# Kernel tuning notes

Hardware: AMD Instinct MI355X
Metric: run time of the kernel (lower is better)

Reference implementation:

```python
import jax, jax.numpy as jnp
import numpy as np

N_NODES = 50000


def setup_inputs() -> dict:
    key = jax.random.key(0)
    k1, k2, k3, k4 = jax.random.split(key, 4)
    in_c, hid = 256, 128
    x = jax.random.normal(k1, (N_NODES, in_c), dtype=jnp.float32)
    edge_index = jax.random.randint(k2, (2, 800000), 0, N_NODES, dtype=jnp.int32)
    # GCNConv weight (glorot) and bias
    W_conv = jax.random.normal(k3, (in_c, hid), dtype=jnp.float32) * (1.0 / np.sqrt(in_c))
    b_conv = jnp.zeros((hid,), dtype=jnp.float32)
    # Final Linear (xavier_uniform per reset_parameters)
    limit = np.sqrt(6.0 / (hid + in_c))
    W_lin = jax.random.uniform(k4, (hid, in_c), dtype=jnp.float32, minval=-limit, maxval=limit)
    b_lin = jnp.zeros((in_c,), dtype=jnp.float32)
    return {"x": x, "edge_index": edge_index, "W_conv": W_conv, "b_conv": b_conv,
            "W_lin": W_lin, "b_lin": b_lin}


def _gcn_conv(x, edge_index, W, b):
    n = x.shape[0]
    # add self-loops (standard GCN normalization)
    loop = jnp.arange(n, dtype=edge_index.dtype)
    src = jnp.concatenate([edge_index[0], loop])
    dst = jnp.concatenate([edge_index[1], loop])
    # transform first (in_c -> hid) so the edge gather moves the smaller dim
    h = x @ W  # [N, hid]
    deg = jax.ops.segment_sum(jnp.ones_like(dst, dtype=h.dtype), dst, num_segments=n)
    dinv = jnp.where(deg > 0, jax.lax.rsqrt(deg), 0.0)
    norm = dinv[src] * dinv[dst]  # [E+N]
    msg = h[src] * norm[:, None]  # [E+N, hid]
    out = jax.ops.segment_sum(msg, dst, num_segments=n)
    return out + b


def reference(x, edge_index, W_conv, b_conv, W_lin, b_lin):
    h = _gcn_conv(x, edge_index, W_conv, b_conv)  # [N, hid]
    # dropout p=0.0 -> identity
    return h @ W_lin + b_lin  # [N, in_c]
```

## Files before the change

kernel.cpp:

```cpp
#include <hip/hip_runtime.h>
#include <hip/hip_fp16.h>


#define N_NODES 50000
#define N_EDGES 800000
#define IN_C 256
#define HID 128
#define SCAN_BLOCKS ((N_NODES + 255) / 256)
#define GEMM_MBLK ((N_NODES + 63) / 64)
#define PREP_BLOCKS 1024
#define BUCKET_BLOCKS 2048
#define LDK 72

#define OFF_H    0UL
#define OFF_CONV 12800000UL
#define OFF_DEG  25600000UL
#define OFF_RP   25800000UL
#define OFF_DINV 26000064UL
#define OFF_RANK 26200064UL
#define OFF_REC  27800064UL
#define OFF_BSUM 31000064UL
#define OFF_WT1  31001088UL
#define OFF_WT2  31066624UL

typedef __attribute__((ext_vector_type(8))) short bf16x8;
typedef __attribute__((ext_vector_type(4))) float f32x4;

__device__ __forceinline__ ushort f2bf(float x) {
    unsigned u = __float_as_uint(x);
    u += 0x7fffu + ((u >> 16) & 1u);
    return (ushort)(u >> 16);
}

__global__ __launch_bounds__(256) void prep_kernel(
    const float* __restrict__ Wc, const float* __restrict__ Wl,
    ushort* __restrict__ wtc, ushort* __restrict__ wtl,
    const int* __restrict__ dst, ushort* __restrict__ rank, int* __restrict__ deg)
{
    int i = blockIdx.x * 256 + threadIdx.x;
    if (i < HID * IN_C) {
        int n = i / IN_C, k = i % IN_C;
        wtc[i] = f2bf(Wc[k * HID + n]);
    } else if (i < 2 * HID * IN_C) {
        int j = i - HID * IN_C;
        int n = j / HID, k = j % HID;
        wtl[j] = f2bf(Wl[k * IN_C + n]);
    }
    for (int e = i; e < N_EDGES; e += PREP_BLOCKS * 256)
        rank[e] = (ushort)atomicAdd(&deg[dst[e]], 1);
}

__global__ __launch_bounds__(256) void scan_blocks_kernel(
    const int* __restrict__ deg, int* __restrict__ row_ptr,
    int* __restrict__ bsums, int n)
{
    __shared__ int tmp[256];
    int tid = threadIdx.x;
    int i = blockIdx.x * 256 + tid;
    int v = (i < n) ? deg[i] : 0;
    int orig = v;
    tmp[tid] = v;
    __syncthreads();
    #pragma unroll
    for (int off = 1; off < 256; off <<= 1) {
        int t = (tid >= off) ? tmp[tid - off] : 0;
        __syncthreads();
        tmp[tid] += t;
        __syncthreads();
    }
    if (i < n) row_ptr[i] = tmp[tid] - orig;
    if (tid == 255) bsums[blockIdx.x] = tmp[255];
}

__global__ __launch_bounds__(256) void finalize2_kernel(
    const int* __restrict__ deg, int* __restrict__ row_ptr,
    const int* __restrict__ bsums, float* __restrict__ dinv, int n)
{
    __shared__ int tmp[256];
    __shared__ int orig[256];
    int tid = threadIdx.x;
    int v = (tid < SCAN_BLOCKS) ? bsums[tid] : 0;
    tmp[tid] = v;
    orig[tid] = v;
    __syncthreads();
    #pragma unroll
    for (int off = 1; off < 256; off <<= 1) {
        int t = (tid >= off) ? tmp[tid - off] : 0;
        __syncthreads();
        tmp[tid] += t;
        __syncthreads();
    }
    int boff = tmp[blockIdx.x] - orig[blockIdx.x];
    int i = blockIdx.x * 256 + tid;
    if (i < n) {
        row_ptr[i] += boff;
        dinv[i] = rsqrtf((float)(deg[i] + 1));
    }
    if (i == 0) row_ptr[n] = N_EDGES;
}

__global__ __launch_bounds__(256) void bucket_kernel(
    const int* __restrict__ src, const int* __restrict__ dst,
    const ushort* __restrict__ rank, const int* __restrict__ row_ptr,
    const float* __restrict__ dinv, unsigned* __restrict__ rec)
{
    int cls = blockIdx.x & 7;
    int blk = blockIdx.x >> 3;
    int lo = cls * (N_NODES / 8);
    int hi = lo + (N_NODES / 8);
    const int CHUNK = (N_EDGES + 255) / 256;
    int e0 = blk * CHUNK;
    int e1 = min(e0 + CHUNK, N_EDGES);
    for (int i = e0 + threadIdx.x; i < e1; i += 256) {
        int d = dst[i];
        if (d >= lo && d < hi) {
            int s = src[i];
            unsigned r = (unsigned)(ushort)s |
                         ((unsigned)__half_as_ushort(__float2half_rn(dinv[s])) << 16);
            rec[row_ptr[d] + rank[i]] = r;
        }
    }
}

template <int KT, bool A_IS_BF16, bool BF16OUT>
__global__ __launch_bounds__(256) void mfma_gemm_kernel(
    const void* __restrict__ Av, const ushort* __restrict__ Bt,
    const float* __restrict__ bias, void* __restrict__ Cv,
    int M, int N)
{
    constexpr int NIT = KT / 64;
    __shared__ __align__(16) ushort As[64 * LDK];
    __shared__ __align__(16) ushort Bs[128 * LDK];
    int tid = threadIdx.x;
    int wave = tid >> 6, lane = tid & 63;
    int quad = lane >> 4, l16 = lane & 15;
    int wm0 = (wave >> 1) * 32, wn0 = (wave & 1) * 64;
    int bm = blockIdx.x * 64, bn = blockIdx.y * 128;

    int arow = tid >> 2, acol = (tid & 3) * 16;
    int agrow = bm + arow;
    int brow = tid >> 1, bkk = (tid & 1) * 32;

    f32x4 acc[2][4] = {};
    float4 a32[2][4];
    bf16x8 a16[2][2];
    bf16x8 breg[2][4];

    auto issue = [&](int it, int s) {
        int k0 = it * 64;
        if (A_IS_BF16) {
            a16[s][0] = bf16x8{};
            a16[s][1] = bf16x8{};
            if (agrow < M) {
                const ushort* ap = (const ushort*)Av + (size_t)agrow * KT + k0 + acol;
                a16[s][0] = *(const bf16x8*)ap;
                a16[s][1] = *(const bf16x8*)(ap + 8);
            }
        } else {
            a32[s][0] = a32[s][1] = a32[s][2] = a32[s][3] = make_float4(0.f, 0.f, 0.f, 0.f);
            if (agrow < M) {
                const float* ap = (const float*)Av + (size_t)agrow * KT + k0 + acol;
                a32[s][0] = *(const float4*)ap;
                a32[s][1] = *(const float4*)(ap + 4);
                a32[s][2] = *(const float4*)(ap + 8);
                a32[s][3] = *(const float4*)(ap + 12);
            }
        }
        const ushort* bp = Bt + (size_t)(bn + brow) * KT + k0 + bkk;
        breg[s][0] = *(const bf16x8*)bp;
        breg[s][1] = *(const bf16x8*)(bp + 8);
        breg[s][2] = *(const bf16x8*)(bp + 16);
        breg[s][3] = *(const bf16x8*)(bp + 24);
    };

    auto stage = [&](int s) {
        if (A_IS_BF16) {
            *(bf16x8*)&As[arow * LDK + acol]     = a16[s][0];
            *(bf16x8*)&As[arow * LDK + acol + 8] = a16[s][1];
        } else {
            ushort t0[8] = {f2bf(a32[s][0].x), f2bf(a32[s][0].y), f2bf(a32[s][0].z), f2bf(a32[s][0].w),
                            f2bf(a32[s][1].x), f2bf(a32[s][1].y), f2bf(a32[s][1].z), f2bf(a32[s][1].w)};
            ushort t1[8] = {f2bf(a32[s][2].x), f2bf(a32[s][2].y), f2bf(a32[s][2].z), f2bf(a32[s][2].w),
                            f2bf(a32[s][3].x), f2bf(a32[s][3].y), f2bf(a32[s][3].z), f2bf(a32[s][3].w)};
            *(bf16x8*)&As[arow * LDK + acol]     = *(bf16x8*)t0;
            *(bf16x8*)&As[arow * LDK + acol + 8] = *(bf16x8*)t1;
        }
        *(bf16x8*)&Bs[brow * LDK + bkk]      = breg[s][0];
        *(bf16x8*)&Bs[brow * LDK + bkk + 8]  = breg[s][1];
        *(bf16x8*)&Bs[brow * LDK + bkk + 16] = breg[s][2];
        *(bf16x8*)&Bs[brow * LDK + bkk + 24] = breg[s][3];
    };

    issue(0, 0);
    #pragma unroll
    for (int it = 0; it < NIT; ++it) {
        int cur = it & 1;
        if (it + 1 < NIT) issue(it + 1, cur ^ 1);
        if (it > 0) __syncthreads();
        stage(cur);
        __syncthreads();
        bf16x8 af[2][2], bfr[4][2];
        #pragma unroll
        for (int im = 0; im < 2; ++im)
            #pragma unroll
            for (int kh = 0; kh < 2; ++kh)
                af[im][kh] = *(bf16x8*)&As[(wm0 + im * 16 + l16) * LDK + kh * 32 + quad * 8];
        #pragma unroll
        for (int in = 0; in < 4; ++in)
            #pragma unroll
            for (int kh = 0; kh < 2; ++kh)
                bfr[in][kh] = *(bf16x8*)&Bs[(wn0 + in * 16 + l16) * LDK + kh * 32 + quad * 8];
        #pragma unroll
        for (int im = 0; im < 2; ++im)
            #pragma unroll
            for (int in = 0; in < 4; ++in) {
                acc[im][in] = __builtin_amdgcn_mfma_f32_16x16x32_bf16(
                    af[im][0], bfr[in][0], acc[im][in], 0, 0, 0);
                acc[im][in] = __builtin_amdgcn_mfma_f32_16x16x32_bf16(
                    af[im][1], bfr[in][1], acc[im][in], 0, 0, 0);
            }
    }
    #pragma unroll
    for (int im = 0; im < 2; ++im) {
        #pragma unroll
        for (int in = 0; in < 4; ++in) {
            int col = bn + wn0 + in * 16 + l16;
            float bval = bias ? bias[col] : 0.f;
            #pragma unroll
            for (int r = 0; r < 4; ++r) {
                int grow = bm + wm0 + im * 16 + quad * 4 + r;
                if (grow < M) {
                    float o = acc[im][in][r] + bval;
                    if (BF16OUT)
                        ((ushort*)Cv)[(size_t)grow * N + col] = f2bf(o);
                    else
                        ((float*)Cv)[(size_t)grow * N + col] = o;
                }
            }
        }
    }
}

__device__ __forceinline__ void acc_edge(float4& acc, unsigned r,
                                         const ushort* __restrict__ hb, int c) {
    unsigned s = r & 0xffffu;
    float w = __half2float(__ushort_as_half((ushort)(r >> 16)));
    uint2 v = *(const uint2*)&hb[(size_t)s * HID + c];
    acc.x += w * __uint_as_float(v.x << 16);
    acc.y += w * __uint_as_float(v.x & 0xffff0000u);
    acc.z += w * __uint_as_float(v.y << 16);
    acc.w += w * __uint_as_float(v.y & 0xffff0000u);
}

__global__ __launch_bounds__(256, 4) void gather_kernel(
    const ushort* __restrict__ hb, const int* __restrict__ row_ptr,
    const unsigned* __restrict__ rec, const float* __restrict__ dinv,
    const float* __restrict__ b_conv, ushort* __restrict__ convb, int n)
{
    int wave = threadIdx.x >> 6;
    int lane = threadIdx.x & 63;
    int d = blockIdx.x * 4 + wave;
    if (d >= n) return;
    int half = lane >> 5;
    int l32 = lane & 31;
    int c = l32 << 2;

    float4 acc = make_float4(0.f, 0.f, 0.f, 0.f);
    int begin = row_ptr[d], end = row_ptr[d + 1];
    int e = begin + half;
    for (; e + 14 < end; e += 16) {
        unsigned r0 = rec[e];
        unsigned r1 = rec[e + 2];
        unsigned r2 = rec[e + 4];
        unsigned r3 = rec[e + 6];
        unsigned r4 = rec[e + 8];
        unsigned r5 = rec[e + 10];
        unsigned r6 = rec[e + 12];
        unsigned r7 = rec[e + 14];
        acc_edge(acc, r0, hb, c);
        acc_edge(acc, r1, hb, c);
        acc_edge(acc, r2, hb, c);
        acc_edge(acc, r3, hb, c);
        acc_edge(acc, r4, hb, c);
        acc_edge(acc, r5, hb, c);
        acc_edge(acc, r6, hb, c);
        acc_edge(acc, r7, hb, c);
    }
    for (; e + 6 < end; e += 8) {
        unsigned r0 = rec[e];
        unsigned r1 = rec[e + 2];
        unsigned r2 = rec[e + 4];
        unsigned r3 = rec[e + 6];
        acc_edge(acc, r0, hb, c);
        acc_edge(acc, r1, hb, c);
        acc_edge(acc, r2, hb, c);
        acc_edge(acc, r3, hb, c);
    }
    for (; e < end; e += 2) {
        unsigned r0 = rec[e];
        acc_edge(acc, r0, hb, c);
    }
    acc.x += __shfl_xor(acc.x, 32);
    acc.y += __shfl_xor(acc.y, 32);
    acc.z += __shfl_xor(acc.z, 32);
    acc.w += __shfl_xor(acc.w, 32);

    if (half == 0) {
        float di = dinv[d];
        uint2 hv = *(const uint2*)&hb[(size_t)d * HID + c];
        acc.x += di * __uint_as_float(hv.x << 16);
        acc.y += di * __uint_as_float(hv.x & 0xffff0000u);
        acc.z += di * __uint_as_float(hv.y << 16);
        acc.w += di * __uint_as_float(hv.y & 0xffff0000u);
        float4 bb = *(const float4*)&b_conv[c];
        float ox = di * acc.x + bb.x;
        float oy = di * acc.y + bb.y;
        float oz = di * acc.z + bb.z;
        float ow = di * acc.w + bb.w;
        uint2 po;
        po.x = ((unsigned)f2bf(oy) << 16) | (unsigned)f2bf(ox);
        po.y = ((unsigned)f2bf(ow) << 16) | (unsigned)f2bf(oz);
        *(uint2*)&convb[(size_t)d * HID + c] = po;
    }
}

extern "C" void kernel_launch(void* const* d_in, const int* in_sizes, int n_in,
                              void* d_out, int out_size, void* d_ws, size_t ws_size,
                              hipStream_t stream) {
    const float* x      = (const float*)d_in[0];
    const int*   ei     = (const int*)d_in[1];
    const float* W_conv = (const float*)d_in[2];
    const float* b_conv = (const float*)d_in[3];
    const float* W_lin  = (const float*)d_in[4];
    const float* b_lin  = (const float*)d_in[5];
    float* out = (float*)d_out;

    char* ws = (char*)d_ws;
    ushort* hb      = (ushort*)(ws + OFF_H);
    ushort* convb   = (ushort*)(ws + OFF_CONV);
    int*    deg     = (int*)(ws + OFF_DEG);
    int*    row_ptr = (int*)(ws + OFF_RP);
    float*  dinv    = (float*)(ws + OFF_DINV);
    ushort* rank    = (ushort*)(ws + OFF_RANK);
    unsigned* rec   = (unsigned*)(ws + OFF_REC);
    int*    bsums   = (int*)(ws + OFF_BSUM);
    ushort* wt_conv = (ushort*)(ws + OFF_WT1);
    ushort* wt_lin  = (ushort*)(ws + OFF_WT2);

    const int* src = ei;
    const int* dst = ei + N_EDGES;

    hipMemsetAsync(deg, 0, 200000, stream);

    prep_kernel<<<PREP_BLOCKS, 256, 0, stream>>>(W_conv, W_lin, wt_conv, wt_lin,
                                                 dst, rank, deg);
    scan_blocks_kernel<<<SCAN_BLOCKS, 256, 0, stream>>>(deg, row_ptr, bsums, N_NODES);
    finalize2_kernel<<<SCAN_BLOCKS, 256, 0, stream>>>(deg, row_ptr, bsums, dinv, N_NODES);

    bucket_kernel<<<BUCKET_BLOCKS, 256, 0, stream>>>(src, dst, rank, row_ptr, dinv, rec);

    mfma_gemm_kernel<IN_C, false, true><<<dim3(GEMM_MBLK, HID / 128), 256, 0, stream>>>(
        x, wt_conv, nullptr, hb, N_NODES, HID);

    gather_kernel<<<(N_NODES + 3) / 4, 256, 0, stream>>>(
        hb, row_ptr, rec, dinv, b_conv, convb, N_NODES);

    mfma_gemm_kernel<HID, true, false><<<dim3(GEMM_MBLK, IN_C / 128), 256, 0, stream>>>(
        convb, wt_lin, b_lin, out, N_NODES, IN_C);
}
```

Baseline: 229.9 us.

## Fuse degree scan, finalize and bucket into one CSR-building kernel

Replaces the two-kernel block scan plus bucket kernel with one csr_kernel. Each block redundantly computes the prefix sum for its 1/8 node class in shared memory, then scatters edge records using the shared-memory row pointers. The dinv array is dropped and rsqrt(deg+1) is recomputed on the fly. This removes two launches and the global row_ptr and dinv round trips. The cost is that every one of the 2048 blocks redundantly re-reads and reduces up to 50000 degrees.

```diff
diff --git a/kernel.cpp b/kernel.cpp
--- a/kernel.cpp
+++ b/kernel.cpp
@@ -6,10 +6,10 @@
 #define N_EDGES 800000
 #define IN_C 256
 #define HID 128
-#define SCAN_BLOCKS ((N_NODES + 255) / 256)
 #define GEMM_MBLK ((N_NODES + 63) / 64)
 #define PREP_BLOCKS 1024
-#define BUCKET_BLOCKS 2048
+#define CSR_BLOCKS 2048
+#define CSIZE (N_NODES / 8)
 #define LDK 72
 
 #define OFF_H    0UL
@@ -50,16 +50,40 @@
         rank[e] = (ushort)atomicAdd(&deg[dst[e]], 1);
 }
 
-__global__ __launch_bounds__(256) void scan_blocks_kernel(
-    const int* __restrict__ deg, int* __restrict__ row_ptr,
-    int* __restrict__ bsums, int n)
+__global__ __launch_bounds__(256) void csr_kernel(
+    const int* __restrict__ src, const int* __restrict__ dst,
+    const ushort* __restrict__ rank, const int* __restrict__ deg,
+    int* __restrict__ row_ptr, unsigned* __restrict__ rec)
 {
+    __shared__ int rp[CSIZE];
     __shared__ int tmp[256];
     int tid = threadIdx.x;
-    int i = blockIdx.x * 256 + tid;
-    int v = (i < n) ? deg[i] : 0;
-    int orig = v;
-    tmp[tid] = v;
+    int cls = blockIdx.x & 7;
+    int blk = blockIdx.x >> 3;
+    int lo = cls * CSIZE;
+
+    int sum = 0;
+    for (int i = tid; i < lo; i += 256) sum += deg[i];
+    tmp[tid] = sum;
+    __syncthreads();
+    #pragma unroll
+    for (int off = 128; off > 0; off >>= 1) {
+        if (tid < off) tmp[tid] += tmp[tid + off];
+        __syncthreads();
+    }
+    int base = tmp[0];
+    __syncthreads();
+
+    int vals[25];
+    int tsum = 0;
+    if (tid < 250) {
+        #pragma unroll
+        for (int j = 0; j < 25; ++j) {
+            vals[j] = deg[lo + tid * 25 + j];
+            tsum += vals[j];
+        }
+    }
+    tmp[tid] = tsum;
     __syncthreads();
     #pragma unroll
     for (int off = 1; off < 256; off <<= 1) {
@@ -68,56 +92,34 @@
         tmp[tid] += t;
         __syncthreads();
     }
-    if (i < n) row_ptr[i] = tmp[tid] - orig;
-    if (tid == 255) bsums[blockIdx.x] = tmp[255];
-}
-
-__global__ __launch_bounds__(256) void finalize2_kernel(
-    const int* __restrict__ deg, int* __restrict__ row_ptr,
-    const int* __restrict__ bsums, float* __restrict__ dinv, int n)
-{
-    __shared__ int tmp[256];
-    __shared__ int orig[256];
-    int tid = threadIdx.x;
-    int v = (tid < SCAN_BLOCKS) ? bsums[tid] : 0;
-    tmp[tid] = v;
-    orig[tid] = v;
+    int run = base + tmp[tid] - tsum;
+    if (tid < 250) {
+        #pragma unroll
+        for (int j = 0; j < 25; ++j) {
+            rp[tid * 25 + j] = run;
+            run += vals[j];
+        }
+    }
     __syncthreads();
-    #pragma unroll
-    for (int off = 1; off < 256; off <<= 1) {
-        int t = (tid >= off) ? tmp[tid - off] : 0;
-        __syncthreads();
-        tmp[tid] += t;
-        __syncthreads();
-    }
-    int boff = tmp[blockIdx.x] - orig[blockIdx.x];
-    int i = blockIdx.x * 256 + tid;
-    if (i < n) {
-        row_ptr[i] += boff;
-        dinv[i] = rsqrtf((float)(deg[i] + 1));
-    }
-    if (i == 0) row_ptr[n] = N_EDGES;
-}
-
-__global__ __launch_bounds__(256) void bucket_kernel(
-    const int* __restrict__ src, const int* __restrict__ dst,
-    const ushort* __restrict__ rank, const int* __restrict__ row_ptr,
-    const float* __restrict__ dinv, unsigned* __restrict__ rec)
-{
-    int cls = blockIdx.x & 7;
-    int blk = blockIdx.x >> 3;
-    int lo = cls * (N_NODES / 8);
-    int hi = lo + (N_NODES / 8);
-    const int CHUNK = (N_EDGES + 255) / 256;
+
+    if (blk == 0) {
+        for (int i = tid; i < CSIZE; i += 256)
+            row_ptr[lo + i] = rp[i];
+        if (cls == 7 && tid == 0) row_ptr[N_NODES] = N_EDGES;
+    }
+
+    const int CHUNK = N_EDGES / 256;
     int e0 = blk * CHUNK;
-    int e1 = min(e0 + CHUNK, N_EDGES);
-    for (int i = e0 + threadIdx.x; i < e1; i += 256) {
+    int e1 = e0 + CHUNK;
+    for (int i = e0 + tid; i < e1; i += 256) {
         int d = dst[i];
-        if (d >= lo && d < hi) {
+        unsigned rel = (unsigned)(d - lo);
+        if (rel < (unsigned)CSIZE) {
             int s = src[i];
+            float dis = rsqrtf((float)(deg[s] + 1));
             unsigned r = (unsigned)(ushort)s |
-                         ((unsigned)__half_as_ushort(__float2half_rn(dinv[s])) << 16);
-            rec[row_ptr[d] + rank[i]] = r;
+                         ((unsigned)__half_as_ushort(__float2half_rn(dis)) << 16);
+            rec[rp[rel] + rank[i]] = r;
         }
     }
 }
@@ -254,7 +256,7 @@
 
 __global__ __launch_bounds__(256, 4) void gather_kernel(
     const ushort* __restrict__ hb, const int* __restrict__ row_ptr,
-    const unsigned* __restrict__ rec, const float* __restrict__ dinv,
+    const unsigned* __restrict__ rec, const int* __restrict__ deg,
     const float* __restrict__ b_conv, ushort* __restrict__ convb, int n)
 {
     int wave = threadIdx.x >> 6;
@@ -306,7 +308,7 @@
     acc.w += __shfl_xor(acc.w, 32);
 
     if (half == 0) {
-        float di = dinv[d];
+        float di = rsqrtf((float)(deg[d] + 1));
         uint2 hv = *(const uint2*)&hb[(size_t)d * HID + c];
         acc.x += di * __uint_as_float(hv.x << 16);
         acc.y += di * __uint_as_float(hv.x & 0xffff0000u);
@@ -340,10 +342,8 @@
     ushort* convb   = (ushort*)(ws + OFF_CONV);
     int*    deg     = (int*)(ws + OFF_DEG);
     int*    row_ptr = (int*)(ws + OFF_RP);
-    float*  dinv    = (float*)(ws + OFF_DINV);
     ushort* rank    = (ushort*)(ws + OFF_RANK);
     unsigned* rec   = (unsigned*)(ws + OFF_REC);
-    int*    bsums   = (int*)(ws + OFF_BSUM);
     ushort* wt_conv = (ushort*)(ws + OFF_WT1);
     ushort* wt_lin  = (ushort*)(ws + OFF_WT2);
 
@@ -354,16 +354,14 @@
 
     prep_kernel<<<PREP_BLOCKS, 256, 0, stream>>>(W_conv, W_lin, wt_conv, wt_lin,
                                                  dst, rank, deg);
-    scan_blocks_kernel<<<SCAN_BLOCKS, 256, 0, stream>>>(deg, row_ptr, bsums, N_NODES);
-    finalize2_kernel<<<SCAN_BLOCKS, 256, 0, stream>>>(deg, row_ptr, bsums, dinv, N_NODES);
-
-    bucket_kernel<<<BUCKET_BLOCKS, 256, 0, stream>>>(src, dst, rank, row_ptr, dinv, rec);
+
+    csr_kernel<<<CSR_BLOCKS, 256, 0, stream>>>(src, dst, rank, deg, row_ptr, rec);
 
     mfma_gemm_kernel<IN_C, false, true><<<dim3(GEMM_MBLK, HID / 128), 256, 0, stream>>>(
         x, wt_conv, nullptr, hb, N_NODES, HID);
 
     gather_kernel<<<(N_NODES + 3) / 4, 256, 0, stream>>>(
-        hb, row_ptr, rec, dinv, b_conv, convb, N_NODES);
+        hb, row_ptr, rec, deg, b_conv, convb, N_NODES);
 
     mfma_gemm_kernel<HID, true, false><<<dim3(GEMM_MBLK, IN_C / 128), 256, 0, stream>>>(
         convb, wt_lin, b_lin, out, N_NODES, IN_C);
```

Result: slower. 267.5 us (+16.4%).
